# Kernel optimization log

Measured on AMD Instinct MI355X. Metric: run time of the kernel, lower is better.

Reference implementation:

```python
import jax, jax.numpy as jnp
import numpy as np

B, S, D, H = 4, 2048, 1024, 16
DK = D // H
THETA = 10000.0


def _rope(x, pos):
    # x: [..., S, DK]; interleaved-pair rotation as in the torch module
    dk = x.shape[-1]
    inv_freq = 1.0 / (THETA ** (jnp.arange(0, dk, 2, dtype=jnp.float32) / dk))  # [dk/2]
    freqs = pos.astype(jnp.float32)[:, None] * inv_freq  # [S, dk/2]
    cos, sin = jnp.cos(freqs), jnp.sin(freqs)
    xr = x.reshape(*x.shape[:-1], dk // 2, 2)
    x0, x1 = xr[..., 0], xr[..., 1]
    rot = jnp.stack([x0 * cos - x1 * sin, x0 * sin + x1 * cos], axis=-1)
    return rot.reshape(x.shape)


def setup_inputs() -> dict:
    key = jax.random.key(0)
    ks = jax.random.split(key, 5)
    scale = 0.02
    return {
        "x": jax.random.normal(ks[0], (B, S, D), dtype=jnp.float32),
        "Wq": jax.random.normal(ks[1], (D, D), dtype=jnp.float32) * scale,
        "Wk": jax.random.normal(ks[2], (D, D), dtype=jnp.float32) * scale,
        "Wv": jax.random.normal(ks[3], (D, D), dtype=jnp.float32) * scale,
        "Wo": jax.random.normal(ks[4], (D, D), dtype=jnp.float32) * scale,
    }


def reference(x, Wq, Wk, Wv, Wo):
    b, s, d = x.shape
    pos = jnp.arange(s)
    # projections (Linear with no bias, y = x @ W^T)
    q = jnp.einsum('bsd,ed->bse', x, Wq).reshape(b, s, H, DK).transpose(0, 2, 1, 3)
    k = jnp.einsum('bsd,ed->bse', x, Wk).reshape(b, s, H, DK).transpose(0, 2, 1, 3)
    v = jnp.einsum('bsd,ed->bse', x, Wv).reshape(b, s, H, DK).transpose(0, 2, 1, 3)
    q = _rope(q, pos)
    k = _rope(k, pos)
    scores = jnp.einsum('bhqd,bhkd->bhqk', q, k) / jnp.sqrt(jnp.float32(DK))
    causal = jnp.tril(jnp.ones((s, s), dtype=bool))
    scores = jnp.where(causal, scores, -jnp.inf)
    attn = jax.nn.softmax(scores, axis=-1)
    out = jnp.einsum('bhqk,bhkd->bhqd', attn, v)
    out = out.transpose(0, 2, 1, 3).reshape(b, s, d)
    return jnp.einsum('bsd,ed->bse', out, Wo)
```

## Files before the change

### kernel.cpp

```cpp
#include <hip/hip_runtime.h>

#define B_  4
#define S_  2048
#define D_  1024
#define H_  16
#define DK_ 64
#define BH_ (B_*H_)
#define L2E 1.44269504088896f

typedef __attribute__((ext_vector_type(8))) short bf16x8;
typedef __attribute__((ext_vector_type(4))) float f32x4;
typedef __attribute__((ext_vector_type(16))) float f32x16;
typedef __attribute__((ext_vector_type(4))) unsigned u32x4;
typedef unsigned short u16;

__device__ __forceinline__ u16 f2bf(float f){
  unsigned u = __builtin_bit_cast(unsigned, f);
  u += 0x7fffu + ((u >> 16) & 1u);
  return (u16)(u >> 16);
}
__device__ __forceinline__ float bf2f(u16 h){
  unsigned u = ((unsigned)h) << 16;
  return __builtin_bit_cast(float, u);
}

#define GLD16(g,l) __builtin_amdgcn_global_load_lds( \
    (const __attribute__((address_space(1))) void*)(g), \
    (__attribute__((address_space(3))) void*)(l), 16, 0, 0)

#define MFMA16(a,b,c) __builtin_amdgcn_mfma_f32_16x16x32_bf16((a),(b),(c),0,0,0)
#define MFMA32(a,b,c) __builtin_amdgcn_mfma_f32_32x32x16_bf16((a),(b),(c),0,0,0)

__global__ void cast_kernel(const float4* __restrict__ in, ushort4* __restrict__ out, int n4){
  int i = blockIdx.x*blockDim.x + threadIdx.x;
  int stride = gridDim.x*blockDim.x;
  for (; i < n4; i += stride){
    float4 v = in[i];
    ushort4 o;
    o.x = f2bf(v.x); o.y = f2bf(v.y); o.z = f2bf(v.z); o.w = f2bf(v.w);
    out[i] = o;
  }
}

__global__ void cast4_kernel(const float4* __restrict__ w0, const float4* __restrict__ w1,
                             const float4* __restrict__ w2, const float4* __restrict__ w3,
                             ushort4* __restrict__ out){
  const int per = D_*D_/4;
  int i = blockIdx.x*blockDim.x + threadIdx.x;
  int stride = gridDim.x*blockDim.x;
  for (; i < 4*per; i += stride){
    int m = i / per, r = i - m*per;
    const float4* src = (m==0)?w0:(m==1)?w1:(m==2)?w2:w3;
    float4 v = src[r];
    ushort4 o;
    o.x = f2bf(v.x); o.y = f2bf(v.y); o.z = f2bf(v.z); o.w = f2bf(v.w);
    out[i] = o;
  }
}

__global__ void trig_kernel(float* __restrict__ ct, float* __restrict__ st){
  int t = blockIdx.x*blockDim.x + threadIdx.x;
  int i = t & 31, s = t >> 5;
  float expo = -(float)(2*i) * (1.0f/(float)DK_);
  float inv = powf(10000.0f, expo);
  float ang = (float)s * inv;
  ct[t] = cosf(ang);
  st[t] = sinf(ang);
}

template<int MODE>
__global__ __launch_bounds__(256, 2)
void gemm_bt(const u16* __restrict__ A,
             const u16* __restrict__ B0, const u16* __restrict__ B1, const u16* __restrict__ B2,
             u16* __restrict__ O0, u16* __restrict__ O1, u16* __restrict__ O2,
             float* __restrict__ Cf,
             const float* __restrict__ ct, const float* __restrict__ st, int K){
  __shared__ __align__(16) u16 lAB[2*128*64];
  u16* const lA = lAB;
  u16* const lB = lAB + 128*64;

  const int id = (int)blockIdx.x;
  const int nchunk = (MODE==0) ? 192 : 64;
  const int swz = (id & 7)*nchunk + (id >> 3);
  int z = 0, rem = swz;
  if (MODE == 0){ z = swz >> 9; rem = swz & 511; }
  const int m0 = (rem >> 3) * 128, n0 = (rem & 7) * 128;

  const u16* Bm = B0;
  u16* Om = O0;
  if (MODE == 0){
    if (z == 1){ Bm = B1; Om = O1; }
    else if (z == 2){ Bm = B2; Om = O2; }
  }
  const int tid = threadIdx.x, wave = tid>>6, lane = tid&63;
  const int wm = wave>>1, wn = wave&1;
  const int srow = lane>>3, scol = (lane&7)*8;

  f32x4 acc[4][4];
  #pragma unroll
  for (int m=0;m<4;++m)
    #pragma unroll
    for (int n=0;n<4;++n) acc[m][n] = (f32x4){0.f,0.f,0.f,0.f};

  #pragma unroll 1
  for (int k0 = 0; k0 < K; k0 += 64){
    #pragma unroll
    for (int j=0;j<4;++j){
      int rb = (wave*4 + j)*8;
      GLD16(A  + (size_t)(m0 + rb + srow)*K + k0 + scol, lA + rb*64);
      GLD16(Bm + (size_t)(n0 + rb + srow)*K + k0 + scol, lB + rb*64);
    }
    __syncthreads();
    #pragma unroll
    for (int kk=0;kk<2;++kk){
      bf16x8 af[4], bfr[4];
      #pragma unroll
      for (int m=0;m<4;++m) af[m]  = *(const bf16x8*)&lA[(wm*64 + m*16 + (lane&15))*64 + kk*32 + (lane>>4)*8];
      #pragma unroll
      for (int n=0;n<4;++n) bfr[n] = *(const bf16x8*)&lB[(wn*64 + n*16 + (lane&15))*64 + kk*32 + (lane>>4)*8];
      #pragma unroll
      for (int m=0;m<4;++m)
        #pragma unroll
        for (int n=0;n<4;++n)
          acc[m][n] = MFMA16(af[m], bfr[n], acc[m][n]);
    }
    __syncthreads();
  }

  if (MODE == 0 && z != 2){
    const float scale = (z == 0) ? 0.125f : 1.0f;
    #pragma unroll
    for (int m=0;m<4;++m){
      const int lr0 = wm*64 + m*16 + ((lane>>4)<<2);
      #pragma unroll
      for (int n=0;n<4;++n){
        const int lc = wn*64 + n*16 + (lane&15);
        #pragma unroll
        for (int r=0;r<4;++r){
          const int lr = lr0 + r;
          lAB[lr*128 + (lc ^ (((lr>>2)&7)<<4))] = f2bf(acc[m][n][r]);
        }
      }
    }
    __syncthreads();
    #pragma unroll
    for (int k=0;k<8;++k){
      const int cid = k*256 + tid;
      const int rr = cid >> 4, cc = cid & 15;
      bf16x8 v = *(const bf16x8*)&lAB[rr*128 + ((cc*8) ^ (((rr>>2)&7)<<4))];
      const int i = m0 + rr, bb = i >> 11, s = i & (S_-1);
      const int e0 = n0 + cc*8, h = e0 >> 6, dk0 = e0 & 63;
      const float4 c4 = *(const float4*)(ct + s*32 + (dk0>>1));
      const float4 s4 = *(const float4*)(st + s*32 + (dk0>>1));
      const float cc4[4] = {c4.x,c4.y,c4.z,c4.w};
      const float ss4[4] = {s4.x,s4.y,s4.z,s4.w};
      bf16x8 o;
      #pragma unroll
      for (int j=0;j<4;++j){
        const float x0 = bf2f((u16)v[2*j]);
        const float x1 = bf2f((u16)v[2*j+1]);
        o[2*j]   = (short)f2bf((x0*cc4[j] - x1*ss4[j])*scale);
        o[2*j+1] = (short)f2bf((x0*ss4[j] + x1*cc4[j])*scale);
      }
      *(bf16x8*)(Om + ((size_t)((bb*H_ + h)*S_ + s))*DK_ + dk0) = o;
    }
  } else {
    #pragma unroll
    for (int m=0;m<4;++m){
      const int rb = m0 + wm*64 + m*16 + ((lane>>4)<<2);
      #pragma unroll
      for (int n=0;n<4;++n){
        const int e = n0 + wn*64 + n*16 + (lane&15);
        if (MODE == 0){
          const int h = e>>6, dk = e&63;
          const int b = rb >> 11, s0 = rb & (S_-1);
          ushort4 w4;
          w4.x = f2bf(acc[m][n][0]); w4.y = f2bf(acc[m][n][1]);
          w4.z = f2bf(acc[m][n][2]); w4.w = f2bf(acc[m][n][3]);
          *(ushort4*)(Om + ((size_t)((b*H_ + h)*DK_ + dk))*S_ + s0) = w4;
        } else {
          #pragma unroll
          for (int r=0;r<4;++r)
            Cf[(size_t)(rb + r)*D_ + e] = acc[m][n][r];
        }
      }
    }
  }
}

__global__ __launch_bounds__(256, 4)
void attn_kernel(const u16* __restrict__ Q, const u16* __restrict__ K,
                 const u16* __restrict__ Vt, u16* __restrict__ O){
  __shared__ __align__(16) u16 lK[2][64*64];
  __shared__ __align__(16) u16 lV[2][64*64];

  const int bh = blockIdx.x;
  const int qt = (int)(gridDim.y - 1 - blockIdx.y);
  const int b = bh >> 4, h = bh & 15;
  const int tid = threadIdx.x, wave = tid>>6, lane = tid&63;
  const int hi = lane >> 5, l31 = lane & 31;
  const int q0 = qt*128, qw = q0 + wave*32;
  const int qg = qw + l31;
  const u16* Qb = Q  + (size_t)bh*S_*DK_;
  const u16* Kb = K  + (size_t)bh*S_*DK_;
  const u16* Vb = Vt + (size_t)bh*DK_*S_;

  bf16x8 qf[4];
  #pragma unroll
  for (int ds=0; ds<4; ++ds)
    qf[ds] = *(const bf16x8*)(Qb + (size_t)qg*DK_ + ds*16 + hi*8);

  f32x16 oacc[2];
  oacc[0] = (f32x16)0.f; oacc[1] = (f32x16)0.f;
  float m_run = -1e30f, l_run = 0.f;

  const int srow8 = lane >> 3;
  const int csw = ((lane&7) ^ srow8) << 3;

  const int kv_end = (qt+1)*128;

  #pragma unroll
  for (int it=0; it<2; ++it){
    const int rb = (it*4 + wave)*8;
    const int row = rb + srow8;
    GLD16(Kb + (size_t)row*DK_ + csw, lK[0] + rb*64);
    GLD16(Vb + (size_t)row*S_ + csw,  lV[0] + rb*64);
  }
  __syncthreads();

  int cur = 0;
  for (int kv0 = 0; kv0 < kv_end; kv0 += 64){
    const int nxt = kv0 + 64;
    if (nxt < kv_end){
      #pragma unroll
      for (int it=0; it<2; ++it){
        const int rb = (it*4 + wave)*8;
        const int row = rb + srow8;
        GLD16(Kb + (size_t)(nxt+row)*DK_ + csw, lK[cur^1] + rb*64);
        GLD16(Vb + (size_t)row*S_ + nxt + csw,  lV[cur^1] + rb*64);
      }
    }

    if (kv0 < qw + 32){
      f32x16 sacc[2];
      sacc[0] = (f32x16)0.f; sacc[1] = (f32x16)0.f;
      __builtin_amdgcn_s_setprio(1);
      #pragma unroll
      for (int kb=0; kb<2; ++kb){
        const int krow = kb*32 + l31;
        #pragma unroll
        for (int ds=0; ds<4; ++ds){
          bf16x8 kf = *(const bf16x8*)&lK[cur][krow*64 + (((ds*2+hi) ^ (krow&7))<<3)];
          sacc[kb] = MFMA32(kf, qf[ds], sacc[kb]);
        }
      }
      __builtin_amdgcn_s_setprio(0);

      if (kv0 + 63 > qw){
        #pragma unroll
        for (int kb=0; kb<2; ++kb)
          #pragma unroll
          for (int r=0; r<16; ++r){
            const int kvg = kv0 + kb*32 + 4*hi + (r&3) + 8*(r>>2);
            if (kvg > qg) sacc[kb][r] = -1e30f;
          }
      }

      float mx = sacc[0][0];
      #pragma unroll
      for (int r=1; r<16; ++r) mx = fmaxf(mx, sacc[0][r]);
      #pragma unroll
      for (int r=0; r<16; ++r) mx = fmaxf(mx, sacc[1][r]);
      mx = fmaxf(mx, __shfl_xor(mx, 32));
      if (!__all((mx - m_run)*L2E <= 8.0f)){
        const float mn = fmaxf(m_run, mx);
        const float alpha = exp2f((m_run - mn)*L2E);
        m_run = mn;
        l_run *= alpha;
        oacc[0] *= alpha;
        oacc[1] *= alpha;
      }
      const float nc = m_run * L2E;
      float ps = 0.f;
      #pragma unroll
      for (int kb=0; kb<2; ++kb)
        #pragma unroll
        for (int r=0; r<16; ++r){
          float v = exp2f(__builtin_fmaf(sacc[kb][r], L2E, -nc));
          sacc[kb][r] = v;
          ps += v;
        }
      ps += __shfl_xor(ps, 32);
      l_run += ps;

      bf16x8 pa[4];
      #pragma unroll
      for (int kb=0; kb<2; ++kb){
        unsigned w[8];
        #pragma unroll
        for (int i=0; i<8; ++i){
          float a = sacc[kb][2*i], b2 = sacc[kb][2*i+1];
          asm("v_cvt_pk_bf16_f32 %0, %1, %2" : "=v"(w[i]) : "v"(a), "v"(b2));
        }
        auto s02 = __builtin_amdgcn_permlane32_swap(w[0], w[2], false, false);
        auto s13 = __builtin_amdgcn_permlane32_swap(w[1], w[3], false, false);
        auto s46 = __builtin_amdgcn_permlane32_swap(w[4], w[6], false, false);
        auto s57 = __builtin_amdgcn_permlane32_swap(w[5], w[7], false, false);
        u32x4 ua = {s02[0], s13[0], s02[1], s13[1]};
        u32x4 ub = {s46[0], s57[0], s46[1], s57[1]};
        pa[kb*2+0] = __builtin_bit_cast(bf16x8, ua);
        pa[kb*2+1] = __builtin_bit_cast(bf16x8, ub);
      }

      __builtin_amdgcn_s_setprio(1);
      #pragma unroll
      for (int dkb=0; dkb<2; ++dkb){
        const int vrow = dkb*32 + l31;
        #pragma unroll
        for (int ks=0; ks<4; ++ks){
          bf16x8 vf = *(const bf16x8*)&lV[cur][vrow*64 + (((ks*2+hi) ^ (vrow&7))<<3)];
          oacc[dkb] = MFMA32(vf, pa[ks], oacc[dkb]);
        }
      }
      __builtin_amdgcn_s_setprio(0);
    }
    __syncthreads();
    cur ^= 1;
  }

  const float inv = 1.0f / l_run;
  #pragma unroll
  for (int dkb=0; dkb<2; ++dkb)
    #pragma unroll
    for (int rq=0; rq<4; ++rq){
      ushort4 w4;
      w4.x = f2bf(oacc[dkb][rq*4+0]*inv);
      w4.y = f2bf(oacc[dkb][rq*4+1]*inv);
      w4.z = f2bf(oacc[dkb][rq*4+2]*inv);
      w4.w = f2bf(oacc[dkb][rq*4+3]*inv);
      const int dk0 = dkb*32 + 8*rq + 4*hi;
      *(ushort4*)(O + (size_t)(b*S_+qg)*D_ + h*DK_ + dk0) = w4;
    }
}

extern "C" void kernel_launch(void* const* d_in, const int* in_sizes, int n_in,
                              void* d_out, int out_size, void* d_ws, size_t ws_size,
                              hipStream_t stream){
  const float* x  = (const float*)d_in[0];
  const float* Wq = (const float*)d_in[1];
  const float* Wk = (const float*)d_in[2];
  const float* Wv = (const float*)d_in[3];
  const float* Wo = (const float*)d_in[4];
  float* out = (float*)d_out;
  char* ws = (char*)d_ws;

  size_t off = 0;
  u16* xb  = (u16*)(ws + off); off += (size_t)B_*S_*D_*2;
  u16* wqb = (u16*)(ws + off); off += (size_t)D_*D_*2;
  u16* wkb = (u16*)(ws + off); off += (size_t)D_*D_*2;
  u16* wvb = (u16*)(ws + off); off += (size_t)D_*D_*2;
  u16* wob = (u16*)(ws + off); off += (size_t)D_*D_*2;
  u16* Qb  = (u16*)(ws + off); off += (size_t)BH_*S_*DK_*2;
  u16* Kb  = (u16*)(ws + off); off += (size_t)BH_*S_*DK_*2;
  u16* Vtb = (u16*)(ws + off); off += (size_t)BH_*S_*DK_*2;
  u16* Ob  = (u16*)(ws + off); off += (size_t)B_*S_*D_*2;
  float* ct = (float*)(ws + off); off += (size_t)S_*32*4;
  float* st = (float*)(ws + off); off += (size_t)S_*32*4;

  cast_kernel<<<2048,256,0,stream>>>((const float4*)x,  (ushort4*)xb,  B_*S_*D_/4);
  cast4_kernel<<<1024,256,0,stream>>>((const float4*)Wq, (const float4*)Wk,
                                      (const float4*)Wv, (const float4*)Wo, (ushort4*)wqb);
  trig_kernel<<<(S_*32)/256,256,0,stream>>>(ct, st);

  gemm_bt<0><<<1536,256,0,stream>>>(xb, wqb,wkb,wvb, Qb,Kb,Vtb, nullptr, ct, st, D_);

  attn_kernel<<<dim3(BH_, S_/128),256,0,stream>>>(Qb, Kb, Vtb, Ob);

  gemm_bt<1><<<512,256,0,stream>>>(Ob, wob,wob,wob, nullptr,nullptr,nullptr, out, nullptr, nullptr, D_);
}
```

Measured before the change: 183.4 us.

## Merge prep kernels and enlarge QKV GEMM tile to 256x128 with swizzled LDS

Folds the three preprocessing launches (x cast, weight cast, RoPE tables) into one kernel to cut launch overhead. Splits the GEMM into a dedicated QKV kernel and an output kernel. The QKV kernel uses 512 threads with a 256x128 tile and an XOR-swizzled LDS layout to reduce bank conflicts and raise operand reuse. Its RoPE epilogue runs in two halves through shared memory. The larger tile needs more LDS and gives fewer blocks, which may lower occupancy or leave CUs idle at the tail.

Result: slower. 243.5 us (+32.7%).

```diff
diff --git a/kernel.cpp b/kernel.cpp
--- a/kernel.cpp
+++ b/kernel.cpp
@@ -31,67 +31,181 @@
 #define MFMA16(a,b,c) __builtin_amdgcn_mfma_f32_16x16x32_bf16((a),(b),(c),0,0,0)
 #define MFMA32(a,b,c) __builtin_amdgcn_mfma_f32_32x32x16_bf16((a),(b),(c),0,0,0)
 
-__global__ void cast_kernel(const float4* __restrict__ in, ushort4* __restrict__ out, int n4){
-  int i = blockIdx.x*blockDim.x + threadIdx.x;
-  int stride = gridDim.x*blockDim.x;
-  for (; i < n4; i += stride){
-    float4 v = in[i];
-    ushort4 o;
-    o.x = f2bf(v.x); o.y = f2bf(v.y); o.z = f2bf(v.z); o.w = f2bf(v.w);
-    out[i] = o;
-  }
-}
-
-__global__ void cast4_kernel(const float4* __restrict__ w0, const float4* __restrict__ w1,
-                             const float4* __restrict__ w2, const float4* __restrict__ w3,
-                             ushort4* __restrict__ out){
-  const int per = D_*D_/4;
-  int i = blockIdx.x*blockDim.x + threadIdx.x;
-  int stride = gridDim.x*blockDim.x;
-  for (; i < 4*per; i += stride){
-    int m = i / per, r = i - m*per;
-    const float4* src = (m==0)?w0:(m==1)?w1:(m==2)?w2:w3;
-    float4 v = src[r];
-    ushort4 o;
-    o.x = f2bf(v.x); o.y = f2bf(v.y); o.z = f2bf(v.z); o.w = f2bf(v.w);
-    out[i] = o;
-  }
-}
-
-__global__ void trig_kernel(float* __restrict__ ct, float* __restrict__ st){
-  int t = blockIdx.x*blockDim.x + threadIdx.x;
-  int i = t & 31, s = t >> 5;
-  float expo = -(float)(2*i) * (1.0f/(float)DK_);
-  float inv = powf(10000.0f, expo);
-  float ang = (float)s * inv;
-  ct[t] = cosf(ang);
-  st[t] = sinf(ang);
-}
-
-template<int MODE>
+__global__ void prep_kernel(const float4* __restrict__ x,
+                            const float4* __restrict__ w0, const float4* __restrict__ w1,
+                            const float4* __restrict__ w2, const float4* __restrict__ w3,
+                            ushort4* __restrict__ xb, ushort4* __restrict__ wb,
+                            float* __restrict__ ct, float* __restrict__ st){
+  const int bid = blockIdx.x;
+  if (bid < 2048){
+    const int n4 = B_*S_*D_/4;
+    int i = bid*blockDim.x + threadIdx.x;
+    for (; i < n4; i += 2048*256){
+      float4 v = x[i];
+      ushort4 o;
+      o.x = f2bf(v.x); o.y = f2bf(v.y); o.z = f2bf(v.z); o.w = f2bf(v.w);
+      xb[i] = o;
+    }
+  } else if (bid < 3072){
+    const int per = D_*D_/4;
+    int i = (bid-2048)*blockDim.x + threadIdx.x;
+    for (; i < 4*per; i += 1024*256){
+      int m = i / per, r = i - m*per;
+      const float4* src = (m==0)?w0:(m==1)?w1:(m==2)?w2:w3;
+      float4 v = src[r];
+      ushort4 o;
+      o.x = f2bf(v.x); o.y = f2bf(v.y); o.z = f2bf(v.z); o.w = f2bf(v.w);
+      wb[i] = o;
+    }
+  } else {
+    const int t = (bid-3072)*blockDim.x + threadIdx.x;
+    const int i = t & 31, s = t >> 5;
+    float expo = -(float)(2*i) * (1.0f/(float)DK_);
+    float inv = powf(10000.0f, expo);
+    float ang = (float)s * inv;
+    ct[t] = cosf(ang);
+    st[t] = sinf(ang);
+  }
+}
+
+__global__ __launch_bounds__(512, 4)
+void gemm_qkv(const u16* __restrict__ A,
+              const u16* __restrict__ B0, const u16* __restrict__ B1, const u16* __restrict__ B2,
+              u16* __restrict__ O0, u16* __restrict__ O1, u16* __restrict__ O2,
+              const float* __restrict__ ct, const float* __restrict__ st){
+  __shared__ __align__(16) u16 lds[24576];
+  u16* const lA = lds;
+  u16* const lB = lds + 16384;
+
+  const int id = (int)blockIdx.x;
+  const int swz = (id & 7)*96 + (id >> 3);
+  const int z = swz >> 8;
+  const int rem = swz & 255;
+  const int m0 = (rem >> 3)*256, n0 = (rem & 7)*128;
+
+  const u16* Bm = (z==0) ? B0 : (z==1) ? B1 : B2;
+  u16* Om = (z==0) ? O0 : (z==1) ? O1 : O2;
+
+  const int tid = threadIdx.x, wave = tid>>6, lane = tid&63;
+  const int wm = wave>>1, wn = wave&1;
+  const int l15 = lane & 15, l4 = lane >> 4;
+  const int srow8 = lane >> 3;
+  const int csw = ((lane&7) ^ srow8) << 3;
+
+  f32x4 acc[4][4];
+  #pragma unroll
+  for (int m=0;m<4;++m)
+    #pragma unroll
+    for (int n=0;n<4;++n) acc[m][n] = (f32x4){0.f,0.f,0.f,0.f};
+
+  #pragma unroll 1
+  for (int k0 = 0; k0 < D_; k0 += 64){
+    #pragma unroll
+    for (int j=0;j<4;++j){
+      const int lr = (j*8 + wave)*8;
+      GLD16(A + (size_t)(m0 + lr + srow8)*D_ + k0 + csw, lA + lr*64);
+    }
+    #pragma unroll
+    for (int j=0;j<2;++j){
+      const int lr = (j*8 + wave)*8;
+      GLD16(Bm + (size_t)(n0 + lr + srow8)*D_ + k0 + csw, lB + lr*64);
+    }
+    __syncthreads();
+    #pragma unroll
+    for (int kk=0;kk<2;++kk){
+      bf16x8 af[4], bfr[4];
+      #pragma unroll
+      for (int m=0;m<4;++m){
+        const int row = wm*64 + m*16 + l15;
+        af[m] = *(const bf16x8*)&lA[row*64 + (((kk*4 + l4) ^ (row&7))<<3)];
+      }
+      #pragma unroll
+      for (int n=0;n<4;++n){
+        const int row = wn*64 + n*16 + l15;
+        bfr[n] = *(const bf16x8*)&lB[row*64 + (((kk*4 + l4) ^ (row&7))<<3)];
+      }
+      #pragma unroll
+      for (int m=0;m<4;++m)
+        #pragma unroll
+        for (int n=0;n<4;++n)
+          acc[m][n] = MFMA16(af[m], bfr[n], acc[m][n]);
+    }
+    __syncthreads();
+  }
+
+  if (z != 2){
+    const float scale = (z == 0) ? 0.125f : 1.0f;
+    #pragma unroll 1
+    for (int p=0;p<2;++p){
+      if ((wm>>1) == p){
+        const int wml = wm & 1;
+        #pragma unroll
+        for (int m=0;m<4;++m){
+          const int lr0 = wml*64 + m*16 + (l4<<2);
+          #pragma unroll
+          for (int n=0;n<4;++n){
+            const int lc = wn*64 + n*16 + l15;
+            #pragma unroll
+            for (int r=0;r<4;++r){
+              const int lr = lr0 + r;
+              lds[lr*128 + (lc ^ (((lr>>2)&7)<<4))] = f2bf(acc[m][n][r]);
+            }
+          }
+        }
+      }
+      __syncthreads();
+      #pragma unroll
+      for (int k=0;k<4;++k){
+        const int cid = k*512 + tid;
+        const int rr = cid >> 4, cc = cid & 15;
+        bf16x8 v = *(const bf16x8*)&lds[rr*128 + ((cc*8) ^ (((rr>>2)&7)<<4))];
+        const int i = m0 + p*128 + rr, bb = i >> 11, s = i & (S_-1);
+        const int e0 = n0 + cc*8, h = e0 >> 6, dk0 = e0 & 63;
+        const float4 c4 = *(const float4*)(ct + s*32 + (dk0>>1));
+        const float4 s4 = *(const float4*)(st + s*32 + (dk0>>1));
+        const float cc4[4] = {c4.x,c4.y,c4.z,c4.w};
+        const float ss4[4] = {s4.x,s4.y,s4.z,s4.w};
+        bf16x8 o;
+        #pragma unroll
+        for (int j=0;j<4;++j){
+          const float x0 = bf2f((u16)v[2*j]);
+          const float x1 = bf2f((u16)v[2*j+1]);
+          o[2*j]   = (short)f2bf((x0*cc4[j] - x1*ss4[j])*scale);
+          o[2*j+1] = (short)f2bf((x0*ss4[j] + x1*cc4[j])*scale);
+        }
+        *(bf16x8*)(Om + ((size_t)((bb*H_ + h)*S_ + s))*DK_ + dk0) = o;
+      }
+      __syncthreads();
+    }
+  } else {
+    #pragma unroll
+    for (int m=0;m<4;++m){
+      const int rb = m0 + wm*64 + m*16 + (l4<<2);
+      const int b = rb >> 11, s0 = rb & (S_-1);
+      #pragma unroll
+      for (int n=0;n<4;++n){
+        const int e = n0 + wn*64 + n*16 + l15;
+        const int h = e>>6, dk = e&63;
+        ushort4 w4;
+        w4.x = f2bf(acc[m][n][0]); w4.y = f2bf(acc[m][n][1]);
+        w4.z = f2bf(acc[m][n][2]); w4.w = f2bf(acc[m][n][3]);
+        *(ushort4*)(Om + ((size_t)((b*H_ + h)*DK_ + dk))*S_ + s0) = w4;
+      }
+    }
+  }
+}
+
 __global__ __launch_bounds__(256, 2)
-void gemm_bt(const u16* __restrict__ A,
-             const u16* __restrict__ B0, const u16* __restrict__ B1, const u16* __restrict__ B2,
-             u16* __restrict__ O0, u16* __restrict__ O1, u16* __restrict__ O2,
-             float* __restrict__ Cf,
-             const float* __restrict__ ct, const float* __restrict__ st, int K){
+void gemm_out(const u16* __restrict__ A, const u16* __restrict__ Bw,
+              float* __restrict__ Cf){
   __shared__ __align__(16) u16 lAB[2*128*64];
   u16* const lA = lAB;
   u16* const lB = lAB + 128*64;
 
   const int id = (int)blockIdx.x;
-  const int nchunk = (MODE==0) ? 192 : 64;
-  const int swz = (id & 7)*nchunk + (id >> 3);
-  int z = 0, rem = swz;
-  if (MODE == 0){ z = swz >> 9; rem = swz & 511; }
-  const int m0 = (rem >> 3) * 128, n0 = (rem & 7) * 128;
-
-  const u16* Bm = B0;
-  u16* Om = O0;
-  if (MODE == 0){
-    if (z == 1){ Bm = B1; Om = O1; }
-    else if (z == 2){ Bm = B2; Om = O2; }
-  }
+  const int swz = (id & 7)*64 + (id >> 3);
+  const int m0 = (swz >> 3) * 128, n0 = (swz & 7) * 128;
+
   const int tid = threadIdx.x, wave = tid>>6, lane = tid&63;
   const int wm = wave>>1, wn = wave&1;
   const int srow = lane>>3, scol = (lane&7)*8;
@@ -103,12 +217,12 @@
     for (int n=0;n<4;++n) acc[m][n] = (f32x4){0.f,0.f,0.f,0.f};
 
   #pragma unroll 1
-  for (int k0 = 0; k0 < K; k0 += 64){
+  for (int k0 = 0; k0 < D_; k0 += 64){
     #pragma unroll
     for (int j=0;j<4;++j){
       int rb = (wave*4 + j)*8;
-      GLD16(A  + (size_t)(m0 + rb + srow)*K + k0 + scol, lA + rb*64);
-      GLD16(Bm + (size_t)(n0 + rb + srow)*K + k0 + scol, lB + rb*64);
+      GLD16(A  + (size_t)(m0 + rb + srow)*D_ + k0 + scol, lA + rb*64);
+      GLD16(Bw + (size_t)(n0 + rb + srow)*D_ + k0 + scol, lB + rb*64);
     }
     __syncthreads();
     #pragma unroll
@@ -127,63 +241,15 @@
     __syncthreads();
   }
 
-  if (MODE == 0 && z != 2){
-    const float scale = (z == 0) ? 0.125f : 1.0f;
-    #pragma unroll
-    for (int m=0;m<4;++m){
-      const int lr0 = wm*64 + m*16 + ((lane>>4)<<2);
-      #pragma unroll
-      for (int n=0;n<4;++n){
-        const int lc = wn*64 + n*16 + (lane&15);
-        #pragma unroll
-        for (int r=0;r<4;++r){
-          const int lr = lr0 + r;
-          lAB[lr*128 + (lc ^ (((lr>>2)&7)<<4))] = f2bf(acc[m][n][r]);
-        }
-      }
-    }
-    __syncthreads();
-    #pragma unroll
-    for (int k=0;k<8;++k){
-      const int cid = k*256 + tid;
-      const int rr = cid >> 4, cc = cid & 15;
-      bf16x8 v = *(const bf16x8*)&lAB[rr*128 + ((cc*8) ^ (((rr>>2)&7)<<4))];
-      const int i = m0 + rr, bb = i >> 11, s = i & (S_-1);
-      const int e0 = n0 + cc*8, h = e0 >> 6, dk0 = e0 & 63;
-      const float4 c4 = *(const float4*)(ct + s*32 + (dk0>>1));
-      const float4 s4 = *(const float4*)(st + s*32 + (dk0>>1));
-      const float cc4[4] = {c4.x,c4.y,c4.z,c4.w};
-      const float ss4[4] = {s4.x,s4.y,s4.z,s4.w};
-      bf16x8 o;
-      #pragma unroll
-      for (int j=0;j<4;++j){
-        const float x0 = bf2f((u16)v[2*j]);
-        const float x1 = bf2f((u16)v[2*j+1]);
-        o[2*j]   = (short)f2bf((x0*cc4[j] - x1*ss4[j])*scale);
-        o[2*j+1] = (short)f2bf((x0*ss4[j] + x1*cc4[j])*scale);
-      }
-      *(bf16x8*)(Om + ((size_t)((bb*H_ + h)*S_ + s))*DK_ + dk0) = o;
-    }
-  } else {
-    #pragma unroll
-    for (int m=0;m<4;++m){
-      const int rb = m0 + wm*64 + m*16 + ((lane>>4)<<2);
-      #pragma unroll
-      for (int n=0;n<4;++n){
-        const int e = n0 + wn*64 + n*16 + (lane&15);
-        if (MODE == 0){
-          const int h = e>>6, dk = e&63;
-          const int b = rb >> 11, s0 = rb & (S_-1);
-          ushort4 w4;
-          w4.x = f2bf(acc[m][n][0]); w4.y = f2bf(acc[m][n][1]);
-          w4.z = f2bf(acc[m][n][2]); w4.w = f2bf(acc[m][n][3]);
-          *(ushort4*)(Om + ((size_t)((b*H_ + h)*DK_ + dk))*S_ + s0) = w4;
-        } else {
-          #pragma unroll
-          for (int r=0;r<4;++r)
-            Cf[(size_t)(rb + r)*D_ + e] = acc[m][n][r];
-        }
-      }
+  #pragma unroll
+  for (int m=0;m<4;++m){
+    const int rb = m0 + wm*64 + m*16 + ((lane>>4)<<2);
+    #pragma unroll
+    for (int n=0;n<4;++n){
+      const int e = n0 + wn*64 + n*16 + (lane&15);
+      #pragma unroll
+      for (int r=0;r<4;++r)
+        Cf[(size_t)(rb + r)*D_ + e] = acc[m][n][r];
     }
   }
 }
@@ -367,14 +433,14 @@
   float* ct = (float*)(ws + off); off += (size_t)S_*32*4;
   float* st = (float*)(ws + off); off += (size_t)S_*32*4;
 
-  cast_kernel<<<2048,256,0,stream>>>((const float4*)x,  (ushort4*)xb,  B_*S_*D_/4);
-  cast4_kernel<<<1024,256,0,stream>>>((const float4*)Wq, (const float4*)Wk,
-                                      (const float4*)Wv, (const float4*)Wo, (ushort4*)wqb);
-  trig_kernel<<<(S_*32)/256,256,0,stream>>>(ct, st);
-
-  gemm_bt<0><<<1536,256,0,stream>>>(xb, wqb,wkb,wvb, Qb,Kb,Vtb, nullptr, ct, st, D_);
+  prep_kernel<<<3328,256,0,stream>>>((const float4*)x,
+                                     (const float4*)Wq, (const float4*)Wk,
+                                     (const float4*)Wv, (const float4*)Wo,
+                                     (ushort4*)xb, (ushort4*)wqb, ct, st);
+
+  gemm_qkv<<<768,512,0,stream>>>(xb, wqb,wkb,wvb, Qb,Kb,Vtb, ct, st);
 
   attn_kernel<<<dim3(BH_, S_/128),256,0,stream>>>(Qb, Kb, Vtb, Ob);
 
-  gemm_bt<1><<<512,256,0,stream>>>(Ob, wob,wob,wob, nullptr,nullptr,nullptr, out, nullptr, nullptr, D_);
-}
+  gemm_out<<<512,256,0,stream>>>(Ob, wob, out);
+}
```

## Software-pipeline PV matmul one KV tile behind QK and softmax

Applied to the files above, without the earlier changes.

Defers the P·V MFMA of each KV tile to the next iteration. It then overlaps with that iteration's QK^T MFMAs and softmax exp work, using a triple-buffered V tile in LDS and a deferred rescale of the output accumulator. The row max and row sum become tree and four-way partial reductions to shorten dependency chains. In exchange the kernel needs more LDS for the third V buffer and more live registers (pa, the pending-state flags), which could lower occupancy under launch bounds of 4.

Measured after the change: 207.3 us. +13.0%, slower.

```diff
diff --git a/kernel.cpp b/kernel.cpp
--- a/kernel.cpp
+++ b/kernel.cpp
@@ -192,14 +192,14 @@
 void attn_kernel(const u16* __restrict__ Q, const u16* __restrict__ K,
                  const u16* __restrict__ Vt, u16* __restrict__ O){
   __shared__ __align__(16) u16 lK[2][64*64];
-  __shared__ __align__(16) u16 lV[2][64*64];
+  __shared__ __align__(16) u16 lV[3][64*64];
 
   const int bh = blockIdx.x;
   const int qt = (int)(gridDim.y - 1 - blockIdx.y);
   const int b = bh >> 4, h = bh & 15;
   const int tid = threadIdx.x, wave = tid>>6, lane = tid&63;
   const int hi = lane >> 5, l31 = lane & 31;
-  const int q0 = qt*128, qw = q0 + wave*32;
+  const int qw = qt*128 + wave*32;
   const int qg = qw + l31;
   const u16* Qb = Q  + (size_t)bh*S_*DK_;
   const u16* Kb = K  + (size_t)bh*S_*DK_;
@@ -213,6 +213,10 @@
   f32x16 oacc[2];
   oacc[0] = (f32x16)0.f; oacc[1] = (f32x16)0.f;
   float m_run = -1e30f, l_run = 0.f;
+
+  bf16x8 pa[4];
+  float alpha_p = 1.f;
+  bool resc_p = false, pending = false;
 
   const int srow8 = lane >> 3;
   const int csw = ((lane&7) ^ srow8) << 3;
@@ -229,6 +233,7 @@
   __syncthreads();
 
   int cur = 0;
+  int va = 2, vb = 0, vc = 1;
   for (int kv0 = 0; kv0 < kv_end; kv0 += 64){
     const int nxt = kv0 + 64;
     if (nxt < kv_end){
@@ -237,12 +242,14 @@
         const int rb = (it*4 + wave)*8;
         const int row = rb + srow8;
         GLD16(Kb + (size_t)(nxt+row)*DK_ + csw, lK[cur^1] + rb*64);
-        GLD16(Vb + (size_t)row*S_ + nxt + csw,  lV[cur^1] + rb*64);
-      }
-    }
-
-    if (kv0 < qw + 32){
-      f32x16 sacc[2];
+        GLD16(Vb + (size_t)row*S_ + nxt + csw,  lV[vc] + rb*64);
+      }
+    }
+
+    const bool active = (kv0 < qw + 32);
+    f32x16 sacc[2];
+
+    if (active){
       sacc[0] = (f32x16)0.f; sacc[1] = (f32x16)0.f;
       __builtin_amdgcn_s_setprio(1);
       #pragma unroll
@@ -255,7 +262,28 @@
         }
       }
       __builtin_amdgcn_s_setprio(0);
-
+    }
+
+    if (pending){
+      if (resc_p){ oacc[0] *= alpha_p; oacc[1] *= alpha_p; }
+      const u16* lvp = lV[va];
+      #pragma unroll
+      for (int dkb=0; dkb<2; ++dkb){
+        bf16x8 vf[4];
+        const int vrow = dkb*32 + l31;
+        #pragma unroll
+        for (int ks=0; ks<4; ++ks)
+          vf[ks] = *(const bf16x8*)&lvp[vrow*64 + (((ks*2+hi) ^ (vrow&7))<<3)];
+        __builtin_amdgcn_s_setprio(1);
+        #pragma unroll
+        for (int ks=0; ks<4; ++ks)
+          oacc[dkb] = MFMA32(vf[ks], pa[ks], oacc[dkb]);
+        __builtin_amdgcn_s_setprio(0);
+      }
+      pending = false;
+    }
+
+    if (active){
       if (kv0 + 63 > qw){
         #pragma unroll
         for (int kb=0; kb<2; ++kb)
@@ -266,34 +294,39 @@
           }
       }
 
-      float mx = sacc[0][0];
-      #pragma unroll
-      for (int r=1; r<16; ++r) mx = fmaxf(mx, sacc[0][r]);
-      #pragma unroll
-      for (int r=0; r<16; ++r) mx = fmaxf(mx, sacc[1][r]);
-      mx = fmaxf(mx, __shfl_xor(mx, 32));
+      float mxv[16];
+      #pragma unroll
+      for (int r=0; r<16; ++r) mxv[r] = fmaxf(sacc[0][r], sacc[1][r]);
+      #pragma unroll
+      for (int s2=8; s2>0; s2>>=1)
+        #pragma unroll
+        for (int r=0; r<8; ++r) if (r < s2) mxv[r] = fmaxf(mxv[r], mxv[r+s2]);
+      const float mx = fmaxf(mxv[0], __shfl_xor(mxv[0], 32));
+
+      float alpha = 1.f; bool resc = false;
       if (!__all((mx - m_run)*L2E <= 8.0f)){
         const float mn = fmaxf(m_run, mx);
-        const float alpha = exp2f((m_run - mn)*L2E);
+        alpha = exp2f((m_run - mn)*L2E);
         m_run = mn;
         l_run *= alpha;
-        oacc[0] *= alpha;
-        oacc[1] *= alpha;
-      }
+        resc = true;
+      }
+      alpha_p = alpha; resc_p = resc;
+
       const float nc = m_run * L2E;
-      float ps = 0.f;
+      float ps4[4] = {0.f, 0.f, 0.f, 0.f};
       #pragma unroll
       for (int kb=0; kb<2; ++kb)
         #pragma unroll
         for (int r=0; r<16; ++r){
           float v = exp2f(__builtin_fmaf(sacc[kb][r], L2E, -nc));
           sacc[kb][r] = v;
-          ps += v;
+          ps4[r & 3] += v;
         }
+      float ps = (ps4[0] + ps4[1]) + (ps4[2] + ps4[3]);
       ps += __shfl_xor(ps, 32);
       l_run += ps;
 
-      bf16x8 pa[4];
       #pragma unroll
       for (int kb=0; kb<2; ++kb){
         unsigned w[8];
@@ -311,21 +344,28 @@
         pa[kb*2+0] = __builtin_bit_cast(bf16x8, ua);
         pa[kb*2+1] = __builtin_bit_cast(bf16x8, ub);
       }
-
-      __builtin_amdgcn_s_setprio(1);
-      #pragma unroll
-      for (int dkb=0; dkb<2; ++dkb){
-        const int vrow = dkb*32 + l31;
-        #pragma unroll
-        for (int ks=0; ks<4; ++ks){
-          bf16x8 vf = *(const bf16x8*)&lV[cur][vrow*64 + (((ks*2+hi) ^ (vrow&7))<<3)];
-          oacc[dkb] = MFMA32(vf, pa[ks], oacc[dkb]);
-        }
-      }
-      __builtin_amdgcn_s_setprio(0);
-    }
+      pending = true;
+    }
+
     __syncthreads();
     cur ^= 1;
+    const int tmp = va; va = vb; vb = vc; vc = tmp;
+  }
+
+  if (pending){
+    if (resc_p){ oacc[0] *= alpha_p; oacc[1] *= alpha_p; }
+    const u16* lvp = lV[va];
+    #pragma unroll
+    for (int dkb=0; dkb<2; ++dkb){
+      bf16x8 vf[4];
+      const int vrow = dkb*32 + l31;
+      #pragma unroll
+      for (int ks=0; ks<4; ++ks)
+        vf[ks] = *(const bf16x8*)&lvp[vrow*64 + (((ks*2+hi) ^ (vrow&7))<<3)];
+      #pragma unroll
+      for (int ks=0; ks<4; ++ks)
+        oacc[dkb] = MFMA32(vf[ks], pa[ks], oacc[dkb]);
+    }
   }
 
   const float inv = 1.0f / l_run;
```
